# Optimization experiments

Hardware: AMD Instinct MI355X
Metric: run time of the kernel (lower is better)

The kernel has to match this reference:

```python
import jax, jax.numpy as jnp
import numpy as np

N = 50000      # nodes across all enclosing subgraphs
E = 1200000    # edges
R = 5          # num_relations
NB = 2         # num_bases
D = 64         # num_features == latent_dim per layer
L = 4          # num_layers
B = 1024       # num enclosing subgraphs (one user + one movie each)


def setup_inputs() -> dict:
    key = jax.random.key(0)
    ks = jax.random.split(key, 10)
    # one-hot node-label features; first B nodes are target users (x[:,0]==1),
    # next B nodes are target movies (x[:,1]==1)
    labels = jax.random.randint(ks[0], (N,), 2, D)
    x = jax.nn.one_hot(labels, D, dtype=jnp.float32)
    x = x.at[:B, :].set(0.0).at[:B, 0].set(1.0)
    x = x.at[B:2 * B, :].set(0.0).at[B:2 * B, 1].set(1.0)
    src = jax.random.randint(ks[1], (E,), 0, N)
    dst = jax.random.randint(ks[2], (E,), 0, N)
    etype = jax.random.randint(ks[3], (E,), 0, R)
    s = 1.0 / np.sqrt(D)
    basis = jax.random.normal(ks[4], (L, NB, D, D), dtype=jnp.float32) * s
    comp = jax.random.normal(ks[5], (L, R, NB), dtype=jnp.float32) * s
    root = jax.random.normal(ks[6], (L, D, D), dtype=jnp.float32) * s
    bias = jnp.zeros((L, D), dtype=jnp.float32)
    w1 = jax.random.normal(ks[7], (2 * L * D, 128), dtype=jnp.float32) * (1.0 / np.sqrt(2 * L * D))
    b1 = jnp.zeros((128,), dtype=jnp.float32)
    w2 = jax.random.normal(ks[8], (128, 1), dtype=jnp.float32) * (1.0 / np.sqrt(128))
    b2 = jnp.zeros((1,), dtype=jnp.float32)
    return dict(x=x, basis=basis, comp=comp, root=root, bias=bias,
                w1=w1, b1=b1, w2=w2, b2=b2,
                src=src, dst=dst, etype=etype, num_graphs=B)


def _rgcn(h, src, dst, etype, basis_l, comp_l, root_l, bias_l):
    # PyG RGCNConv with basis decomposition and per-relation mean aggregation.
    n_rel = comp_l.shape[0]
    x_src = h[src]                                # [E, Din] gather
    w_e = comp_l[etype]                           # [E, NB] basis coefficients per edge
    msg = jnp.zeros((src.shape[0], basis_l.shape[-1]), h.dtype)
    for b in range(basis_l.shape[0]):             # NB = 2, fixed small loop
        msg = msg + w_e[:, b:b + 1] * (x_src @ basis_l[b])
    # mean over incoming edges per (dst, relation)
    seg = dst * n_rel + etype
    cnt = jax.ops.segment_sum(jnp.ones((src.shape[0],), h.dtype), seg,
                              num_segments=h.shape[0] * n_rel)
    msg = msg * (1.0 / jnp.maximum(cnt[seg], 1.0))[:, None]
    agg = jax.ops.segment_sum(msg, dst, num_segments=h.shape[0])  # scatter-add
    return agg + h @ root_l + bias_l


def reference(x, basis, comp, root, bias, w1, b1, w2, b2, src, dst, etype, num_graphs):
    h = x
    states = []
    for l in range(basis.shape[0]):               # 4 layers
        h = jnp.tanh(_rgcn(h, src, dst, etype, basis[l], comp[l], root[l], bias[l]))
        states.append(h)
    cat = jnp.concatenate(states, axis=1)         # [N, L*D]
    users = jnp.nonzero(x[:, 0] == 1.0, size=num_graphs)[0]
    movies = jnp.nonzero(x[:, 1] == 1.0, size=num_graphs)[0]
    g = jnp.concatenate([cat[users], cat[movies]], axis=1)  # [B, 2*L*D]
    hid = jax.nn.relu(g @ w1 + b1)                # eval mode: dropout is a no-op
    out = hid @ w2 + b2
    return out[:, 0]
```

## Files before the change

### kernel.cpp

```cpp
#include <hip/hip_runtime.h>
#include <hip/hip_fp16.h>
#include <math.h>

#define D      64
#define L      4
#define R      5
#define BGRAPH 1024
#define CT     4096
#define BK     128
#define INVCAP 4096

typedef __attribute__((ext_vector_type(8))) short short8;
typedef __attribute__((ext_vector_type(8))) _Float16 half8;
typedef __attribute__((ext_vector_type(4))) float f32x4;


__global__ void hist_init_k(const int* __restrict__ dst, int* __restrict__ bh,
                            const float* __restrict__ x, __half* __restrict__ hf,
                            unsigned char* __restrict__ labels,
                            const float* __restrict__ basis, const float* __restrict__ root,
                            ushort* __restrict__ Mhi, ushort* __restrict__ Mlo,
                            int E, int nbl, int nbuck, int N, int nbCopy) {
    if ((int)blockIdx.x < nbl) {
        __shared__ int cnt[392];
        for (int k = threadIdx.x; k < nbuck; k += 256) cnt[k] = 0;
        __syncthreads();
        int base = blockIdx.x * CT;
        int end = base + CT < E ? base + CT : E;
        for (int i = base + threadIdx.x; i < end; i += 256)
            atomicAdd(&cnt[dst[i] >> 7], 1);
        __syncthreads();
        for (int k = threadIdx.x; k < nbuck; k += 256)
            bh[k * nbl + blockIdx.x] = cnt[k];
    } else if ((int)blockIdx.x < nbl + nbCopy) {
        int wid = threadIdx.x >> 6, lane = threadIdx.x & 63;
        int v = (blockIdx.x - nbl) * 4 + wid;
        if (v >= N) return;
        float val = x[(size_t)v * D + lane];
        hf[(size_t)v * D + lane] = __float2half(val);
        unsigned long long m = __ballot(val > 0.5f);
        if (lane == 0) labels[v] = (unsigned char)__builtin_ctzll(m);
    } else {
        int t = (blockIdx.x - nbl - nbCopy) * 256 + threadIdx.x;
        if (t >= L * 4 * 6 * 64 * 8) return;
        int j = t & 7;
        int lane = (t >> 3) & 63;
        int rem = t >> 9;
        int kt = rem % 6;
        int lcg = rem / 6;
        int cg = lcg & 3, l = lcg >> 2;
        int k = kt * 32 + (lane >> 4) * 8 + j;
        int col = cg * 16 + (lane & 15);
        float val;
        if (k < 64)       val = basis[(((size_t)l * 2 + 0) * D + k) * D + col];
        else if (k < 128) val = basis[(((size_t)l * 2 + 1) * D + (k - 64)) * D + col];
        else              val = root[((size_t)l * D + (k - 128)) * D + col];
        __half hi = __float2half(val);
        Mhi[t] = __half_as_ushort(hi);
        Mlo[t] = __half_as_ushort(__float2half(val - __half2float(hi)));
    }
}

__global__ void scan1(const int* __restrict__ hist, int* __restrict__ offs,
                      int* __restrict__ bsums, int n) {
    __shared__ int tmp[256];
    int i = blockIdx.x * 256 + threadIdx.x;
    int v = (i < n) ? hist[i] : 0;
    tmp[threadIdx.x] = v;
    __syncthreads();
    for (int o = 1; o < 256; o <<= 1) {
        int t = 0;
        if (threadIdx.x >= o) t = tmp[threadIdx.x - o];
        __syncthreads();
        if (threadIdx.x >= o) tmp[threadIdx.x] += t;
        __syncthreads();
    }
    if (i < n) offs[i] = tmp[threadIdx.x] - v;
    if (threadIdx.x == 255) bsums[blockIdx.x] = tmp[255];
}

__device__ __forceinline__ void scan_bsums(const int* __restrict__ bsums, int nb,
                                           int* tmp, int* ex) {
    int t = threadIdx.x;
    int v = (t < nb) ? bsums[t] : 0;
    tmp[t] = v;
    __syncthreads();
    for (int o = 1; o < 512; o <<= 1) {
        int tv = 0;
        if (t >= o) tv = tmp[t - o];
        __syncthreads();
        if (t >= o) tmp[t] += tv;
        __syncthreads();
    }
    ex[t] = tmp[t] - v;
    __syncthreads();
}

__global__ __launch_bounds__(512)
void coarse_scatter(const int* __restrict__ dst, const int* __restrict__ src,
                    const int* __restrict__ et, const int* __restrict__ bh,
                    const int* __restrict__ bsums, int* __restrict__ pe,
                    int E, int nbl, int nbuck, int nb) {
    __shared__ int tmp[512];
    __shared__ int ex[512];
    __shared__ int cur[392];
    scan_bsums(bsums, nb, tmp, ex);
    for (int k = threadIdx.x; k < nbuck; k += 512) {
        int idx = k * nbl + blockIdx.x;
        cur[k] = bh[idx] + ex[idx >> 8];
    }
    __syncthreads();
    int base = blockIdx.x * CT;
    int end = base + CT < E ? base + CT : E;
    for (int i = base + threadIdx.x; i < end; i += 512) {
        int d = dst[i];
        int pos = atomicAdd(&cur[d >> 7], 1);
        pe[pos] = src[i] | (et[i] << 16) | ((d & 127) << 19);
    }
}

__global__ __launch_bounds__(512)
void fine_sort(const int* __restrict__ pe, const int* __restrict__ bh,
               const int* __restrict__ bsums, int* __restrict__ offs,
               int* __restrict__ meta, float* __restrict__ invcN,
               int E, int nbl, int N, int nb) {
    __shared__ int tmp[512];
    __shared__ int ex[512];
    __shared__ int cnt[BK];
    __shared__ int pref[BK];
    __shared__ int cur[BK];
    __shared__ int cntR[BK * R];
    __shared__ int inv[INVCAP];
    int b = blockIdx.x, t = threadIdx.x;
    scan_bsums(bsums, nb, tmp, ex);
    int i0 = b * nbl;
    int rbeg = bh[i0] + ex[i0 >> 8];
    int rend;
    if (b == gridDim.x - 1) rend = E;
    else { int i1 = (b + 1) * nbl; rend = bh[i1] + ex[i1 >> 8]; }
    int sz = rend - rbeg;
    if (t < BK) { cnt[t] = 0; cur[t] = 0; }
    for (int k = t; k < BK * R; k += 512) cntR[k] = 0;
    __syncthreads();
    for (int i = rbeg + t; i < rend; i += 512) {
        int pk = pe[i];
        int ln = (pk >> 19) & 127;
        atomicAdd(&cnt[ln], 1);
        atomicAdd(&cntR[ln * R + ((pk >> 16) & 7)], 1);
    }
    __syncthreads();
    if (t < BK) pref[t] = cnt[t];
    __syncthreads();
    for (int o = 1; o < BK; o <<= 1) {
        int tv = 0;
        if (t >= o && t < BK) tv = pref[t - o];
        __syncthreads();
        if (t >= o && t < BK) pref[t] += tv;
        __syncthreads();
    }
    if (t < BK) {
        int node = b * BK + t;
        if (node <= N) offs[node] = rbeg + pref[t] - cnt[t];
    }
    for (int k = t; k < BK * R; k += 512) {
        int c = cntR[k];
        float ic = 1.0f / (float)(c > 0 ? c : 1);
        ((float*)cntR)[k] = ic;
        int node = b * BK + k / R;
        if (node < N) invcN[(size_t)b * BK * R + k] = ic;
    }
    __syncthreads();
    if (sz <= INVCAP) {
        for (int i = rbeg + t; i < rend; i += 512) {
            int pk = pe[i];
            int ln = (pk >> 19) & 127;
            int lp = pref[ln] - cnt[ln] + atomicAdd(&cur[ln], 1);
            inv[lp] = pk;
        }
        __syncthreads();
        for (int k = t; k < sz; k += 512)
            meta[rbeg + k] = inv[k] & 0x7FFFF;
    } else {
        for (int i = rbeg + t; i < rend; i += 512) {
            int pk = pe[i];
            int ln = (pk >> 19) & 127;
            int pos = rbeg + (pref[ln] - cnt[ln]) + atomicAdd(&cur[ln], 1);
            meta[pos] = pk & 0x7FFFF;
        }
    }
}

__global__ __launch_bounds__(256)
void layer_fused(const int* __restrict__ offs, const int* __restrict__ meta,
                 const float* __restrict__ invcN, const unsigned char* __restrict__ labels,
                 const __half* __restrict__ hfin,
                 const ushort* __restrict__ Mhi_l, const ushort* __restrict__ Mlo_l,
                 const float* __restrict__ bias_l, const float* __restrict__ comp_l,
                 __half* __restrict__ hfout, float* __restrict__ g, int l, int N) {
    __shared__ union {
        float  f32[16][132];
        __half f16[16][136];
    } zu;
    __shared__ float2  wnT[16][5];
    __shared__ __half2 wn0[16][5];
    __shared__ __half2 wn1[16][5];
    int tid = threadIdx.x;
    int tile = blockIdx.x;
    int vbase0 = tile * 16;
    if (tid < 16 * R) {
        int n = tid / R, r = tid % R;
        int v = vbase0 + n;
        float ic = (v < N) ? invcN[(size_t)v * R + r] : 0.f;
        float w0f = comp_l[2 * r] * ic, w1f = comp_l[2 * r + 1] * ic;
        wnT[n][r] = make_float2(w0f, w1f);
        wn0[n][r] = __float2half2_rn(w0f);
        wn1[n][r] = __float2half2_rn(w1f);
    }
    int wid = tid >> 6, lane = tid & 63;

    if (l == 0) {
        for (int k = tid; k < 16 * 132; k += 256) ((float*)zu.f32)[k] = 0.f;
        __syncthreads();
        int nl = tid >> 4, sl = tid & 15;
        int v = vbase0 + nl;
        if (v < N) {
            int b = offs[v], e2 = offs[v + 1];
            for (int i = b + sl; i < e2; i += 16) {
                int pk = meta[i];
                int s = pk & 0xFFFF;
                int r = (pk >> 16) & 7;
                float2 wt = wnT[nl][r];
                int lab = labels[s];
                atomicAdd(&zu.f32[nl][lab], wt.x);
                atomicAdd(&zu.f32[nl][64 + lab], wt.y);
            }
        }
    } else {
        __syncthreads();
        int h = lane >> 5;
        int n = (lane >> 3) & 3;
        int q = lane & 7;
        int nl = wid * 4 + n;
        int v = vbase0 + nl;
        bool vlive = v < N;
        int vc = vlive ? v : 0;
        int b = offs[vc];
        int e2 = vlive ? offs[vc + 1] : b;
        int len = e2 - b;
        int lmax = len;
        lmax = max(lmax, __shfl_xor(lmax, 8));
        lmax = max(lmax, __shfl_xor(lmax, 16));
        int nits = (lmax + 1) >> 1;
        __half2 z2 = __float2half2_rn(0.f);
        __half2 a0[4] = { z2, z2, z2, z2 }, a1[4] = { z2, z2, z2, z2 };
        const float4* hf16 = (const float4*)hfin;
        #pragma unroll 4
        for (int it = 0; it < nits; ++it) {
            int e = it * 2 + h;
            bool live = e < len;
            int gi = live ? (b + e) : 0;
            int pk = meta[gi];
            int s = pk & 0xFFFF;
            int r = (pk >> 16) & 7;
            __half2 w0 = wn0[nl][r];
            __half2 w1 = wn1[nl][r];
            if (!live) { w0 = z2; w1 = z2; }
            float4 hv = hf16[(size_t)s * 8 + q];
            const __half2* hp = (const __half2*)&hv;
            #pragma unroll
            for (int k2 = 0; k2 < 4; ++k2) {
                a0[k2] = __hfma2(w0, hp[k2], a0[k2]);
                a1[k2] = __hfma2(w1, hp[k2], a1[k2]);
            }
        }
        #pragma unroll
        for (int k = 0; k < 4; ++k) {
            int ia = *(int*)&a0[k];
            int ib = __shfl_xor(ia, 32);
            a0[k] = __hadd2(a0[k], *(__half2*)&ib);
            ia = *(int*)&a1[k];
            ib = __shfl_xor(ia, 32);
            a1[k] = __hadd2(a1[k], *(__half2*)&ib);
        }
        if (vlive && h == 0) {
            *(short8*)(&zu.f16[nl][8 * q])      = *(short8*)a0;
            *(short8*)(&zu.f16[nl][64 + 8 * q]) = *(short8*)a1;
        }
    }
    __syncthreads();

    int m = lane & 15, lg = lane >> 4;
    int row = vbase0 + m;
    int rowc = row < N ? row : N - 1;
    half8 a[6];
    if (l == 0) {
        #pragma unroll
        for (int kt = 0; kt < 4; ++kt) {
            const float* zp = &zu.f32[m][kt * 32 + lg * 8];
            union { half8 v; __half hh[8]; } A;
            #pragma unroll
            for (int q2 = 0; q2 < 8; ++q2) A.hh[q2] = __float2half(zp[q2]);
            a[kt] = A.v;
        }
    } else {
        #pragma unroll
        for (int kt = 0; kt < 4; ++kt)
            a[kt] = *(const half8*)(&zu.f16[m][kt * 32 + lg * 8]);
    }
    #pragma unroll
    for (int kt = 4; kt < 6; ++kt)
        a[kt] = *(const half8*)(hfin + (size_t)rowc * D + (kt - 4) * 32 + lg * 8);

    int cg = wid;
    int col = cg * 16 + m;
    float bv = bias_l[col];
    f32x4 acc = { bv, bv, bv, bv };
    #pragma unroll
    for (int kt = 0; kt < 4; ++kt) {
        size_t boff = ((size_t)(cg * 6 + kt) * 64 + lane) * 8;
        half8 bhi = *(const half8*)(Mhi_l + boff);
        acc = __builtin_amdgcn_mfma_f32_16x16x32_f16(a[kt], bhi, acc, 0, 0, 0);
    }
    #pragma unroll
    for (int kt = 4; kt < 6; ++kt) {
        size_t boff = ((size_t)(cg * 6 + kt) * 64 + lane) * 8;
        half8 bhi = *(const half8*)(Mhi_l + boff);
        half8 blo = *(const half8*)(Mlo_l + boff);
        acc = __builtin_amdgcn_mfma_f32_16x16x32_f16(a[kt], bhi, acc, 0, 0, 0);
        acc = __builtin_amdgcn_mfma_f32_16x16x32_f16(a[kt], blo, acc, 0, 0, 0);
    }
    int rowbase = vbase0 + lg * 4;
    #pragma unroll
    for (int r = 0; r < 4; ++r) {
        int node = rowbase + r;
        if (node < N) {
            float tv = tanhf(acc[r]);
            hfout[(size_t)node * D + col] = __float2half(tv);
            if (node < BGRAPH)
                g[(size_t)node * (2 * L * D) + l * D + col] = tv;
            else if (node < 2 * BGRAPH)
                g[(size_t)(node - BGRAPH) * (2 * L * D) + L * D + l * D + col] = tv;
        }
    }
}

__global__ void mlp4(const float* __restrict__ g, const float* __restrict__ w1,
                     const float* __restrict__ b1, const float* __restrict__ w2,
                     const float* __restrict__ b2, float* __restrict__ out) {
    __shared__ float gl[4][512];
    __shared__ float red[2][4][128];
    int tid = threadIdx.x;
    int rowbase = blockIdx.x * 4;
    for (int i = tid; i < 4 * 512; i += 256)
        gl[i >> 9][i & 511] = g[(size_t)rowbase * 512 + i];
    __syncthreads();
    int t = tid & 127, kh = tid >> 7;
    float s0 = 0.f, s1 = 0.f, s2 = 0.f, s3 = 0.f;
    int k0 = kh * 256;
    #pragma unroll 4
    for (int k = k0; k < k0 + 256; ++k) {
        float wv = w1[k * 128 + t];
        s0 = fmaf(gl[0][k], wv, s0);
        s1 = fmaf(gl[1][k], wv, s1);
        s2 = fmaf(gl[2][k], wv, s2);
        s3 = fmaf(gl[3][k], wv, s3);
    }
    red[kh][0][t] = s0; red[kh][1][t] = s1; red[kh][2][t] = s2; red[kh][3][t] = s3;
    __syncthreads();
    if (kh == 0) {
        #pragma unroll
        for (int r = 0; r < 4; ++r)
            gl[r][t] = fmaxf(red[0][r][t] + red[1][r][t] + b1[t], 0.f) * w2[t];
    }
    __syncthreads();
    int w = tid >> 6, lane = tid & 63;
    float val = gl[w][lane] + gl[w][lane + 64];
    #pragma unroll
    for (int o = 32; o > 0; o >>= 1) val += __shfl_down(val, o);
    if (lane == 0) out[rowbase + w] = val + b2[0];
}

extern "C" void kernel_launch(void* const* d_in, const int* in_sizes, int n_in,
                              void* d_out, int out_size, void* d_ws, size_t ws_size,
                              hipStream_t stream) {
    const float* x     = (const float*)d_in[0];
    const float* basis = (const float*)d_in[1];
    const float* comp  = (const float*)d_in[2];
    const float* root  = (const float*)d_in[3];
    const float* bias  = (const float*)d_in[4];
    const float* w1    = (const float*)d_in[5];
    const float* b1    = (const float*)d_in[6];
    const float* w2    = (const float*)d_in[7];
    const float* b2    = (const float*)d_in[8];
    const int*   src   = (const int*)d_in[9];
    const int*   dst   = (const int*)d_in[10];
    const int*   et    = (const int*)d_in[11];
    float* out = (float*)d_out;

    const int N = in_sizes[0] / D;
    const int E = in_sizes[9];

    const int nbl = (E + CT - 1) / CT;
    const int nbuck = (N + BK - 1) / BK;
    const int nbh = nbuck * nbl;
    const int nb = (nbh + 255) / 256;

    char* p = (char*)d_ws;
    auto alloc = [&](size_t bytes) -> char* {
        char* q = p;
        p += (bytes + 255) & ~(size_t)255;
        return q;
    };
    int*    offsN = (int*)alloc((size_t)(N + 1) * 4);
    int*    bh    = (int*)alloc((size_t)(nbh + 1) * 4);
    int*    bsums = (int*)alloc(1024 * 4);
    int*    pe    = (int*)alloc((size_t)E * 4);
    int*    meta  = (int*)alloc((size_t)E * 4);
    float*  invcN = (float*)alloc((size_t)(nbuck * BK) * R * 4);
    unsigned char* labels = (unsigned char*)alloc((size_t)N);
    __half* hf0   = (__half*)alloc((size_t)N * D * 2);
    __half* hf1   = (__half*)alloc((size_t)N * D * 2);
    float*  gbuf  = (float*)alloc((size_t)BGRAPH * 2 * L * D * 4);
    ushort* Mhi   = (ushort*)alloc((size_t)L * 4 * 6 * 64 * 8 * 2);
    ushort* Mlo   = (ushort*)alloc((size_t)L * 4 * 6 * 64 * 8 * 2);

    int nbCopy = (N + 3) / 4;
    hist_init_k<<<nbl + nbCopy + 192, 256, 0, stream>>>(
        dst, bh, x, hf0, labels, basis, root, Mhi, Mlo, E, nbl, nbuck, N, nbCopy);
    scan1<<<nb, 256, 0, stream>>>(bh, bh, bsums, nbh);
    coarse_scatter<<<nbl, 512, 0, stream>>>(dst, src, et, bh, bsums, pe,
                                            E, nbl, nbuck, nb);
    fine_sort<<<nbuck, 512, 0, stream>>>(pe, bh, bsums, offsN, meta, invcN,
                                         E, nbl, N, nb);

    __half* hbuf[2] = { hf0, hf1 };
    int lgrid = (N + 15) / 16;
    for (int l = 0; l < L; ++l) {
        layer_fused<<<lgrid, 256, 0, stream>>>(offsN, meta, invcN, labels,
                                               hbuf[l & 1],
                                               Mhi + (size_t)l * 4 * 6 * 64 * 8,
                                               Mlo + (size_t)l * 4 * 6 * 64 * 8,
                                               bias + (size_t)l * D,
                                               comp + (size_t)l * R * 2,
                                               hbuf[(l + 1) & 1], gbuf, l, N);
    }
    mlp4<<<BGRAPH / 4, 256, 0, stream>>>(gbuf, w1, b1, w2, b2, out);
}
```

Baseline: 159.2 us.

## Merge scan, coarse scatter and fine sort into one cooperative kernel

Replaces the three separate launches for the block-sum scan, the coarse bucket scatter and the fine per-node sort with a single cooperative kernel that uses grid.sync() between phases. Shared memory for the scatter and sort phases is unioned. This removes two kernel launch boundaries and their gaps. The cost is grid-wide barriers, and the grid (about 391 blocks of 512 threads, each holding roughly 20 KB of LDS) must be fully co-resident or the cooperative launch fails.

```diff
diff --git a/kernel.cpp b/kernel.cpp
--- a/kernel.cpp
+++ b/kernel.cpp
@@ -1,6 +1,9 @@
 #include <hip/hip_runtime.h>
 #include <hip/hip_fp16.h>
+#include <hip/hip_cooperative_groups.h>
 #include <math.h>
+
+namespace cg = cooperative_groups;
 
 #define D      64
 #define L      4
@@ -61,111 +64,104 @@
     }
 }
 
-__global__ void scan1(const int* __restrict__ hist, int* __restrict__ offs,
-                      int* __restrict__ bsums, int n) {
-    __shared__ int tmp[256];
-    int i = blockIdx.x * 256 + threadIdx.x;
-    int v = (i < n) ? hist[i] : 0;
-    tmp[threadIdx.x] = v;
-    __syncthreads();
-    for (int o = 1; o < 256; o <<= 1) {
-        int t = 0;
-        if (threadIdx.x >= o) t = tmp[threadIdx.x - o];
-        __syncthreads();
-        if (threadIdx.x >= o) tmp[threadIdx.x] += t;
-        __syncthreads();
-    }
-    if (i < n) offs[i] = tmp[threadIdx.x] - v;
-    if (threadIdx.x == 255) bsums[blockIdx.x] = tmp[255];
-}
-
-__device__ __forceinline__ void scan_bsums(const int* __restrict__ bsums, int nb,
-                                           int* tmp, int* ex) {
-    int t = threadIdx.x;
-    int v = (t < nb) ? bsums[t] : 0;
-    tmp[t] = v;
-    __syncthreads();
-    for (int o = 1; o < 512; o <<= 1) {
-        int tv = 0;
-        if (t >= o) tv = tmp[t - o];
-        __syncthreads();
-        if (t >= o) tmp[t] += tv;
-        __syncthreads();
-    }
-    ex[t] = tmp[t] - v;
-    __syncthreads();
-}
-
 __global__ __launch_bounds__(512)
-void coarse_scatter(const int* __restrict__ dst, const int* __restrict__ src,
-                    const int* __restrict__ et, const int* __restrict__ bh,
-                    const int* __restrict__ bsums, int* __restrict__ pe,
-                    int E, int nbl, int nbuck, int nb) {
+void sort_coop(const int* __restrict__ dst, const int* __restrict__ src,
+               const int* __restrict__ et, int* __restrict__ bh,
+               int* __restrict__ bsums, int* __restrict__ pe,
+               int* __restrict__ offs, int* __restrict__ meta,
+               float* __restrict__ invcN,
+               int E, int nbl, int nbuck, int nbh, int nb, int N) {
+    cg::grid_group grid = cg::this_grid();
     __shared__ int tmp[512];
     __shared__ int ex[512];
-    __shared__ int cur[392];
-    scan_bsums(bsums, nb, tmp, ex);
-    for (int k = threadIdx.x; k < nbuck; k += 512) {
-        int idx = k * nbl + blockIdx.x;
-        cur[k] = bh[idx] + ex[idx >> 8];
-    }
-    __syncthreads();
-    int base = blockIdx.x * CT;
-    int end = base + CT < E ? base + CT : E;
-    for (int i = base + threadIdx.x; i < end; i += 512) {
-        int d = dst[i];
-        int pos = atomicAdd(&cur[d >> 7], 1);
-        pe[pos] = src[i] | (et[i] << 16) | ((d & 127) << 19);
-    }
-}
-
-__global__ __launch_bounds__(512)
-void fine_sort(const int* __restrict__ pe, const int* __restrict__ bh,
-               const int* __restrict__ bsums, int* __restrict__ offs,
-               int* __restrict__ meta, float* __restrict__ invcN,
-               int E, int nbl, int N, int nb) {
-    __shared__ int tmp[512];
-    __shared__ int ex[512];
-    __shared__ int cnt[BK];
-    __shared__ int pref[BK];
-    __shared__ int cur[BK];
-    __shared__ int cntR[BK * R];
-    __shared__ int inv[INVCAP];
+    __shared__ union {
+        struct { int cur[392]; } s2;
+        struct { int cnt[BK]; int pref[BK]; int cur[BK]; int cntR[BK * R]; int inv[INVCAP]; } s3;
+    } u;
     int b = blockIdx.x, t = threadIdx.x;
-    scan_bsums(bsums, nb, tmp, ex);
+
+    if (b < nb) {
+        int i = b * 256 + t;
+        int v = 0;
+        if (t < 256) { v = (i < nbh) ? bh[i] : 0; tmp[t] = v; }
+        __syncthreads();
+        for (int o = 1; o < 256; o <<= 1) {
+            int tv = 0;
+            if (t >= o && t < 256) tv = tmp[t - o];
+            __syncthreads();
+            if (t >= o && t < 256) tmp[t] += tv;
+            __syncthreads();
+        }
+        if (t < 256 && i < nbh) bh[i] = tmp[t] - v;
+        if (t == 255) bsums[b] = tmp[255];
+    }
+    grid.sync();
+
+    {
+        int v = (t < nb) ? bsums[t] : 0;
+        tmp[t] = v;
+        __syncthreads();
+        for (int o = 1; o < 512; o <<= 1) {
+            int tv = 0;
+            if (t >= o) tv = tmp[t - o];
+            __syncthreads();
+            if (t >= o) tmp[t] += tv;
+            __syncthreads();
+        }
+        ex[t] = tmp[t] - v;
+        __syncthreads();
+    }
+
+    if (b < nbl) {
+        for (int k = t; k < nbuck; k += 512) {
+            int idx = k * nbl + b;
+            u.s2.cur[k] = bh[idx] + ex[idx >> 8];
+        }
+        __syncthreads();
+        int base = b * CT;
+        int end = base + CT < E ? base + CT : E;
+        for (int i = base + t; i < end; i += 512) {
+            int d = dst[i];
+            int pos = atomicAdd(&u.s2.cur[d >> 7], 1);
+            pe[pos] = src[i] | (et[i] << 16) | ((d & 127) << 19);
+        }
+    }
+    grid.sync();
+
+    if (b >= nbuck) return;
     int i0 = b * nbl;
     int rbeg = bh[i0] + ex[i0 >> 8];
     int rend;
-    if (b == gridDim.x - 1) rend = E;
+    if (b == nbuck - 1) rend = E;
     else { int i1 = (b + 1) * nbl; rend = bh[i1] + ex[i1 >> 8]; }
     int sz = rend - rbeg;
-    if (t < BK) { cnt[t] = 0; cur[t] = 0; }
-    for (int k = t; k < BK * R; k += 512) cntR[k] = 0;
+    if (t < BK) { u.s3.cnt[t] = 0; u.s3.cur[t] = 0; }
+    for (int k = t; k < BK * R; k += 512) u.s3.cntR[k] = 0;
     __syncthreads();
     for (int i = rbeg + t; i < rend; i += 512) {
         int pk = pe[i];
         int ln = (pk >> 19) & 127;
-        atomicAdd(&cnt[ln], 1);
-        atomicAdd(&cntR[ln * R + ((pk >> 16) & 7)], 1);
-    }
-    __syncthreads();
-    if (t < BK) pref[t] = cnt[t];
+        atomicAdd(&u.s3.cnt[ln], 1);
+        atomicAdd(&u.s3.cntR[ln * R + ((pk >> 16) & 7)], 1);
+    }
+    __syncthreads();
+    if (t < BK) u.s3.pref[t] = u.s3.cnt[t];
     __syncthreads();
     for (int o = 1; o < BK; o <<= 1) {
         int tv = 0;
-        if (t >= o && t < BK) tv = pref[t - o];
-        __syncthreads();
-        if (t >= o && t < BK) pref[t] += tv;
+        if (t >= o && t < BK) tv = u.s3.pref[t - o];
+        __syncthreads();
+        if (t >= o && t < BK) u.s3.pref[t] += tv;
         __syncthreads();
     }
     if (t < BK) {
         int node = b * BK + t;
-        if (node <= N) offs[node] = rbeg + pref[t] - cnt[t];
+        if (node <= N) offs[node] = rbeg + u.s3.pref[t] - u.s3.cnt[t];
     }
     for (int k = t; k < BK * R; k += 512) {
-        int c = cntR[k];
+        int c = u.s3.cntR[k];
         float ic = 1.0f / (float)(c > 0 ? c : 1);
-        ((float*)cntR)[k] = ic;
+        ((float*)u.s3.cntR)[k] = ic;
         int node = b * BK + k / R;
         if (node < N) invcN[(size_t)b * BK * R + k] = ic;
     }
@@ -174,17 +170,17 @@
         for (int i = rbeg + t; i < rend; i += 512) {
             int pk = pe[i];
             int ln = (pk >> 19) & 127;
-            int lp = pref[ln] - cnt[ln] + atomicAdd(&cur[ln], 1);
-            inv[lp] = pk;
+            int lp = u.s3.pref[ln] - u.s3.cnt[ln] + atomicAdd(&u.s3.cur[ln], 1);
+            u.s3.inv[lp] = pk;
         }
         __syncthreads();
         for (int k = t; k < sz; k += 512)
-            meta[rbeg + k] = inv[k] & 0x7FFFF;
+            meta[rbeg + k] = u.s3.inv[k] & 0x7FFFF;
     } else {
         for (int i = rbeg + t; i < rend; i += 512) {
             int pk = pe[i];
             int ln = (pk >> 19) & 127;
-            int pos = rbeg + (pref[ln] - cnt[ln]) + atomicAdd(&cur[ln], 1);
+            int pos = rbeg + (u.s3.pref[ln] - u.s3.cnt[ln]) + atomicAdd(&u.s3.cur[ln], 1);
             meta[pos] = pk & 0x7FFFF;
         }
     }
@@ -311,19 +307,19 @@
     for (int kt = 4; kt < 6; ++kt)
         a[kt] = *(const half8*)(hfin + (size_t)rowc * D + (kt - 4) * 32 + lg * 8);
 
-    int cg = wid;
-    int col = cg * 16 + m;
+    int cg2 = wid;
+    int col = cg2 * 16 + m;
     float bv = bias_l[col];
     f32x4 acc = { bv, bv, bv, bv };
     #pragma unroll
     for (int kt = 0; kt < 4; ++kt) {
-        size_t boff = ((size_t)(cg * 6 + kt) * 64 + lane) * 8;
+        size_t boff = ((size_t)(cg2 * 6 + kt) * 64 + lane) * 8;
         half8 bhi = *(const half8*)(Mhi_l + boff);
         acc = __builtin_amdgcn_mfma_f32_16x16x32_f16(a[kt], bhi, acc, 0, 0, 0);
     }
     #pragma unroll
     for (int kt = 4; kt < 6; ++kt) {
-        size_t boff = ((size_t)(cg * 6 + kt) * 64 + lane) * 8;
+        size_t boff = ((size_t)(cg2 * 6 + kt) * 64 + lane) * 8;
         half8 bhi = *(const half8*)(Mhi_l + boff);
         half8 blo = *(const half8*)(Mlo_l + boff);
         acc = __builtin_amdgcn_mfma_f32_16x16x32_f16(a[kt], bhi, acc, 0, 0, 0);
@@ -427,11 +423,21 @@
     int nbCopy = (N + 3) / 4;
     hist_init_k<<<nbl + nbCopy + 192, 256, 0, stream>>>(
         dst, bh, x, hf0, labels, basis, root, Mhi, Mlo, E, nbl, nbuck, N, nbCopy);
-    scan1<<<nb, 256, 0, stream>>>(bh, bh, bsums, nbh);
-    coarse_scatter<<<nbl, 512, 0, stream>>>(dst, src, et, bh, bsums, pe,
-                                            E, nbl, nbuck, nb);
-    fine_sort<<<nbuck, 512, 0, stream>>>(pe, bh, bsums, offsN, meta, invcN,
-                                         E, nbl, N, nb);
+
+    {
+        int ngrid = nb;
+        if (nbl > ngrid) ngrid = nbl;
+        if (nbuck > ngrid) ngrid = nbuck;
+        const int* dstA = dst; const int* srcA = src; const int* etA = et;
+        int* bhA = bh; int* bsumsA = bsums; int* peA = pe;
+        int* offsA = offsN; int* metaA = meta; float* invcA = invcN;
+        int Ea = E, nbla = nbl, nbucka = nbuck, nbha = nbh, nba = nb, Na = N;
+        void* args[] = { &dstA, &srcA, &etA, &bhA, &bsumsA, &peA,
+                         &offsA, &metaA, &invcA,
+                         &Ea, &nbla, &nbucka, &nbha, &nba, &Na };
+        hipLaunchCooperativeKernel((void*)sort_coop, dim3(ngrid), dim3(512),
+                                   args, 0, stream);
+    }
 
     __half* hbuf[2] = { hf0, hf1 };
     int lgrid = (N + 15) / 16;
```

New measurement: 277.0 us. 1.74x slower.
